# Kernel optimization log

Measured on AMD Instinct MI355X. Metric: run time of the kernel, lower is better.

## Reference

```python
import jax, jax.numpy as jnp
import numpy as np
import math

S, D = 8192, 128

def setup_inputs() -> dict:
    key = jax.random.key(0)
    kq, kk, kv = jax.random.split(key, 3)
    return {
        "q": jax.random.normal(kq, (S, D), dtype=jnp.float32),
        "k": jax.random.normal(kk, (S, D), dtype=jnp.float32),
        "v": jax.random.normal(kv, (S, D), dtype=jnp.float32),
    }

def reference(q, k, v):
    # scores: [S, S]; scale by sqrt(d) as in the torch module
    scale = 1.0 / math.sqrt(q.shape[1])
    scores = (q @ k.T) * scale
    attn = jax.nn.softmax(scores, axis=-1)
    return attn @ v
```

## Files before the change

kernel.cpp:

```cpp
#include <hip/hip_runtime.h>
#include <hip/hip_bf16.h>

#define SEQ 8192
#define HD 128
#define BM 128
#define BN 64
#define NQT (SEQ / BM)
#define THREADS 256
#define KTP 130
#define VTP 66
#define PTP 66

typedef __bf16 bf16_t;
typedef __bf16 bf16x8 __attribute__((ext_vector_type(8)));
typedef float f32x4 __attribute__((ext_vector_type(4)));
typedef float f32x16 __attribute__((ext_vector_type(16)));

#if __has_builtin(__builtin_amdgcn_exp2f)
__device__ inline float exp2_fast(float x) { return __builtin_amdgcn_exp2f(x); }
#else
__device__ inline float exp2_fast(float x) { return exp2f(x); }
#endif

__global__ __launch_bounds__(256) void prep_kernel(const float* __restrict__ K,
                                                   const float* __restrict__ V,
                                                   bf16_t* __restrict__ Kb,
                                                   bf16_t* __restrict__ VT) {
  const int b = (int)blockIdx.x;
  const int tid = (int)threadIdx.x;
  if (b < 256) {
    __shared__ float tile[64][65];
    const int s0 = (b & 127) * 64;
    const int d0 = (b >> 7) * 64;
    const int r = tid >> 2;
    const int c0 = (tid & 3) * 16;
#pragma unroll
    for (int j4 = 0; j4 < 4; ++j4) {
      float4 x = *(const float4*)&V[(size_t)(s0 + r) * HD + d0 + c0 + j4 * 4];
      tile[r][c0 + j4 * 4 + 0] = x.x;
      tile[r][c0 + j4 * 4 + 1] = x.y;
      tile[r][c0 + j4 * 4 + 2] = x.z;
      tile[r][c0 + j4 * 4 + 3] = x.w;
    }
    __syncthreads();
    bf16x8 w0, w1;
#pragma unroll
    for (int j = 0; j < 8; ++j) w0[j] = (bf16_t)tile[c0 + j][r];
#pragma unroll
    for (int j = 0; j < 8; ++j) w1[j] = (bf16_t)tile[c0 + 8 + j][r];
    *(bf16x8*)&VT[(size_t)(d0 + r) * SEQ + s0 + c0] = w0;
    *(bf16x8*)&VT[(size_t)(d0 + r) * SEQ + s0 + c0 + 8] = w1;
  } else {
    const int base = (b - 256) * 2048 + tid * 8;
    float4 a = *(const float4*)&K[base];
    float4 c = *(const float4*)&K[base + 4];
    bf16x8 f;
    f[0] = (bf16_t)a.x; f[1] = (bf16_t)a.y; f[2] = (bf16_t)a.z; f[3] = (bf16_t)a.w;
    f[4] = (bf16_t)c.x; f[5] = (bf16_t)c.y; f[6] = (bf16_t)c.z; f[7] = (bf16_t)c.w;
    *(bf16x8*)&Kb[base] = f;
  }
}

__global__ __launch_bounds__(THREADS, 2) void fattn_kernel(
    const float* __restrict__ Q, const bf16_t* __restrict__ Kb,
    const bf16_t* __restrict__ VT, float* __restrict__ Opart,
    float* __restrict__ Lpart, int kshift, int nit) {
  __shared__ __align__(16) bf16_t kt[BN][KTP];
  __shared__ __align__(16) bf16_t vt[HD][VTP];
  __shared__ __align__(16) bf16_t pt[4][32][PTP];

  const int tid = (int)threadIdx.x;
  const int lane = tid & 63;
  const int w = tid >> 6;
  const int h = lane >> 5;
  const int n32 = lane & 31;

  const int qt = (int)blockIdx.x >> kshift;
  const int sp = (int)blockIdx.x & ((1 << kshift) - 1);
  const int qbase = qt * BM;
  const int kbase0 = sp * (nit * BN);

  const float SC2 = 0.08838834764831845f * 1.4426950408889634f;

  const int kr0 = tid >> 4;
  const int kc8 = (tid & 15) * 8;
  const int vd0 = tid >> 3;
  const int vc8 = (tid & 7) * 8;

  bf16x8 qf[8];
  {
    const float* qp = Q + (size_t)(qbase + w * 32 + n32) * HD + h * 8;
#pragma unroll
    for (int kk = 0; kk < 8; ++kk) {
      float4 a = *(const float4*)(qp + kk * 16);
      float4 b = *(const float4*)(qp + kk * 16 + 4);
      bf16x8 f;
      f[0] = (bf16_t)a.x; f[1] = (bf16_t)a.y; f[2] = (bf16_t)a.z; f[3] = (bf16_t)a.w;
      f[4] = (bf16_t)b.x; f[5] = (bf16_t)b.y; f[6] = (bf16_t)b.z; f[7] = (bf16_t)b.w;
      qf[kk] = f;
    }
  }

  f32x16 o_acc[4];
#pragma unroll
  for (int i = 0; i < 4; ++i)
#pragma unroll
    for (int e = 0; e < 16; ++e) o_acc[i][e] = 0.f;
  float l_acc[16];
#pragma unroll
  for (int i = 0; i < 16; ++i) l_acc[i] = 0.f;

  for (int it = 0; it < nit; ++it) {
    const int kbase = kbase0 + it * BN;

    bf16x8 kreg[4], vreg[4];
#pragma unroll
    for (int j = 0; j < 4; ++j)
      kreg[j] = *(const bf16x8*)&Kb[(size_t)(kbase + kr0 + 16 * j) * HD + kc8];
#pragma unroll
    for (int j = 0; j < 4; ++j)
      vreg[j] = *(const bf16x8*)&VT[(size_t)(vd0 + 32 * j) * SEQ + kbase + vc8];

    __syncthreads();
#pragma unroll
    for (int j = 0; j < 4; ++j) *(bf16x8*)&kt[kr0 + 16 * j][kc8] = kreg[j];
#pragma unroll
    for (int j = 0; j < 4; ++j) *(bf16x8*)&vt[vd0 + 32 * j][vc8] = vreg[j];
    __syncthreads();

    f32x16 sacc[2];
#pragma unroll
    for (int nt = 0; nt < 2; ++nt)
#pragma unroll
      for (int e = 0; e < 16; ++e) sacc[nt][e] = 0.f;
#pragma unroll
    for (int kk = 0; kk < 8; ++kk) {
#pragma unroll
      for (int nt = 0; nt < 2; ++nt) {
        bf16x8 b = *(const bf16x8*)&kt[nt * 32 + n32][kk * 16 + h * 8];
        sacc[nt] = __builtin_amdgcn_mfma_f32_32x32x16_bf16(qf[kk], b, sacc[nt], 0, 0, 0);
      }
    }

#pragma unroll
    for (int nt = 0; nt < 2; ++nt) {
#pragma unroll
      for (int reg = 0; reg < 16; ++reg) {
        float p = exp2_fast(sacc[nt][reg] * SC2);
        l_acc[reg] += p;
        const int row = (reg & 3) + 8 * (reg >> 2);
        pt[w][row + 4 * h][nt * 32 + n32] = (bf16_t)p;
      }
    }

#pragma unroll
    for (int kk = 0; kk < 4; ++kk) {
      bf16x8 pa = *(const bf16x8*)&pt[w][n32][kk * 16 + h * 8];
#pragma unroll
      for (int ot = 0; ot < 4; ++ot) {
        bf16x8 vb = *(const bf16x8*)&vt[ot * 32 + n32][kk * 16 + h * 8];
        o_acc[ot] = __builtin_amdgcn_mfma_f32_32x32x16_bf16(pa, vb, o_acc[ot], 0, 0, 0);
      }
    }
  }

  {
    float* op = Opart + ((size_t)sp * SEQ + qbase + w * 32) * HD;
#pragma unroll
    for (int ot = 0; ot < 4; ++ot)
#pragma unroll
      for (int reg = 0; reg < 16; ++reg) {
        const int row = (reg & 3) + 8 * (reg >> 2) + 4 * h;
        op[row * HD + ot * 32 + n32] = o_acc[ot][reg];
      }
#pragma unroll
    for (int reg = 0; reg < 16; ++reg) {
      float v = l_acc[reg];
      v += __shfl_xor(v, 1);
      v += __shfl_xor(v, 2);
      v += __shfl_xor(v, 4);
      v += __shfl_xor(v, 8);
      v += __shfl_xor(v, 16);
      l_acc[reg] = v;
    }
    if (n32 == 0) {
      float* lp = Lpart + (size_t)sp * SEQ + qbase + w * 32;
#pragma unroll
      for (int reg = 0; reg < 16; ++reg)
        lp[(reg & 3) + 8 * (reg >> 2) + 4 * h] = l_acc[reg];
    }
  }
}

__global__ __launch_bounds__(256) void combine_kernel(const float* __restrict__ Opart,
                                                      const float* __restrict__ Lpart,
                                                      float* __restrict__ out, int ksplit) {
  const int tid = (int)threadIdx.x;
  const int row = (int)blockIdx.x * 8 + (tid >> 5);
  const int c0 = (tid & 31) * 4;
  float lsum = 0.f;
  for (int s = 0; s < ksplit; ++s) lsum += Lpart[(size_t)s * SEQ + row];
  f32x4 acc;
#pragma unroll
  for (int e = 0; e < 4; ++e) acc[e] = 0.f;
  for (int s = 0; s < ksplit; ++s) {
    f32x4 o = *(const f32x4*)&Opart[((size_t)s * SEQ + row) * HD + c0];
#pragma unroll
    for (int e = 0; e < 4; ++e) acc[e] += o[e];
  }
  const float inv = 1.0f / lsum;
  f32x4 res;
#pragma unroll
  for (int e = 0; e < 4; ++e) res[e] = acc[e] * inv;
  *(f32x4*)&out[(size_t)row * HD + c0] = res;
}

extern "C" void kernel_launch(void* const* d_in, const int* in_sizes, int n_in,
                              void* d_out, int out_size, void* d_ws, size_t ws_size,
                              hipStream_t stream) {
  const float* Q = (const float*)d_in[0];
  const float* K = (const float*)d_in[1];
  const float* V = (const float*)d_in[2];
  float* out = (float*)d_out;

  int ksplit = 8, kshift = 3;
  while (ksplit > 1) {
    size_t need = (size_t)ksplit * SEQ * HD * 4
                + (size_t)ksplit * SEQ * 4
                + (size_t)SEQ * HD * 2 * 2;
    if (need <= ws_size) break;
    ksplit >>= 1; kshift--;
  }

  char* ws = (char*)d_ws;
  float* Opart = (float*)ws;
  float* Lpart = (float*)(ws + (size_t)ksplit * SEQ * HD * 4);
  bf16_t* Kb = (bf16_t*)(ws + (size_t)ksplit * SEQ * HD * 4 + (size_t)ksplit * SEQ * 4);
  bf16_t* VT = Kb + (size_t)SEQ * HD;

  const int nit = SEQ / (ksplit * BN);

  prep_kernel<<<768, 256, 0, stream>>>(K, V, Kb, VT);
  fattn_kernel<<<NQT * ksplit, THREADS, 0, stream>>>(Q, Kb, VT, Opart, Lpart, kshift, nit);
  combine_kernel<<<SEQ / 8, 256, 0, stream>>>(Opart, Lpart, out, ksplit);
}
```

Before: 122.6 us.

## Double-buffer K/V tiles and keep P in registers via transposed score MFMA

K and V tiles now live in two LDS buffers. The next tile's global loads are issued before the current tile's compute, leaving one barrier per iteration instead of two. The score MFMA swaps its operands to compute K·Q^T, so each lane holds one query's probabilities. These are packed to bf16 and rearranged with a cross-half lane shuffle to form the PV A-operand directly, which removes the LDS round trip for P and shrinks the row-sum to one value per lane. The softmax scale is folded into Q at load time. In exchange the code adds shuffle and select logic, and the doubled K/V buffers raise LDS use, though the P buffer is gone.

```diff
diff --git a/kernel.cpp b/kernel.cpp
--- a/kernel.cpp
+++ b/kernel.cpp
@@ -9,12 +9,13 @@
 #define THREADS 256
 #define KTP 130
 #define VTP 66
-#define PTP 66
 
 typedef __bf16 bf16_t;
+typedef __bf16 bf16x2 __attribute__((ext_vector_type(2)));
 typedef __bf16 bf16x8 __attribute__((ext_vector_type(8)));
 typedef float f32x4 __attribute__((ext_vector_type(4)));
 typedef float f32x16 __attribute__((ext_vector_type(16)));
+typedef unsigned int u32x4 __attribute__((ext_vector_type(4)));
 
 #if __has_builtin(__builtin_amdgcn_exp2f)
 __device__ inline float exp2_fast(float x) { return __builtin_amdgcn_exp2f(x); }
@@ -65,9 +66,8 @@
     const float* __restrict__ Q, const bf16_t* __restrict__ Kb,
     const bf16_t* __restrict__ VT, float* __restrict__ Opart,
     float* __restrict__ Lpart, int kshift, int nit) {
-  __shared__ __align__(16) bf16_t kt[BN][KTP];
-  __shared__ __align__(16) bf16_t vt[HD][VTP];
-  __shared__ __align__(16) bf16_t pt[4][32][PTP];
+  __shared__ __align__(16) bf16_t kts[2][BN][KTP];
+  __shared__ __align__(16) bf16_t vts[2][HD][VTP];
 
   const int tid = (int)threadIdx.x;
   const int lane = tid & 63;
@@ -95,8 +95,10 @@
       float4 a = *(const float4*)(qp + kk * 16);
       float4 b = *(const float4*)(qp + kk * 16 + 4);
       bf16x8 f;
-      f[0] = (bf16_t)a.x; f[1] = (bf16_t)a.y; f[2] = (bf16_t)a.z; f[3] = (bf16_t)a.w;
-      f[4] = (bf16_t)b.x; f[5] = (bf16_t)b.y; f[6] = (bf16_t)b.z; f[7] = (bf16_t)b.w;
+      f[0] = (bf16_t)(a.x * SC2); f[1] = (bf16_t)(a.y * SC2);
+      f[2] = (bf16_t)(a.z * SC2); f[3] = (bf16_t)(a.w * SC2);
+      f[4] = (bf16_t)(b.x * SC2); f[5] = (bf16_t)(b.y * SC2);
+      f[6] = (bf16_t)(b.z * SC2); f[7] = (bf16_t)(b.w * SC2);
       qf[kk] = f;
     }
   }
@@ -106,62 +108,88 @@
   for (int i = 0; i < 4; ++i)
 #pragma unroll
     for (int e = 0; e < 16; ++e) o_acc[i][e] = 0.f;
-  float l_acc[16];
-#pragma unroll
-  for (int i = 0; i < 16; ++i) l_acc[i] = 0.f;
+  float l_acc = 0.f;
+
+  {
+#pragma unroll
+    for (int j = 0; j < 4; ++j) {
+      bf16x8 kr = *(const bf16x8*)&Kb[(size_t)(kbase0 + kr0 + 16 * j) * HD + kc8];
+      *(bf16x8*)&kts[0][kr0 + 16 * j][kc8] = kr;
+    }
+#pragma unroll
+    for (int j = 0; j < 4; ++j) {
+      bf16x8 vr = *(const bf16x8*)&VT[(size_t)(vd0 + 32 * j) * SEQ + kbase0 + vc8];
+      *(bf16x8*)&vts[0][vd0 + 32 * j][vc8] = vr;
+    }
+  }
+  __syncthreads();
 
   for (int it = 0; it < nit; ++it) {
-    const int kbase = kbase0 + it * BN;
-
+    const int cur = it & 1;
+    const int nxt = cur ^ 1;
+    const int nk = (it + 1 < nit) ? kbase0 + (it + 1) * BN : kbase0;
     bf16x8 kreg[4], vreg[4];
 #pragma unroll
     for (int j = 0; j < 4; ++j)
-      kreg[j] = *(const bf16x8*)&Kb[(size_t)(kbase + kr0 + 16 * j) * HD + kc8];
+      kreg[j] = *(const bf16x8*)&Kb[(size_t)(nk + kr0 + 16 * j) * HD + kc8];
 #pragma unroll
     for (int j = 0; j < 4; ++j)
-      vreg[j] = *(const bf16x8*)&VT[(size_t)(vd0 + 32 * j) * SEQ + kbase + vc8];
-
+      vreg[j] = *(const bf16x8*)&VT[(size_t)(vd0 + 32 * j) * SEQ + nk + vc8];
+
+    f32x16 sacc[2];
+#pragma unroll
+    for (int nt = 0; nt < 2; ++nt)
+#pragma unroll
+      for (int e = 0; e < 16; ++e) sacc[nt][e] = 0.f;
+#pragma unroll
+    for (int kk = 0; kk < 8; ++kk) {
+#pragma unroll
+      for (int nt = 0; nt < 2; ++nt) {
+        bf16x8 af = *(const bf16x8*)&kts[cur][nt * 32 + n32][kk * 16 + h * 8];
+        sacc[nt] = __builtin_amdgcn_mfma_f32_32x32x16_bf16(af, qf[kk], sacc[nt], 0, 0, 0);
+      }
+    }
+
+#pragma unroll
+    for (int nt = 0; nt < 2; ++nt) {
+      float pf[16];
+#pragma unroll
+      for (int r = 0; r < 16; ++r) pf[r] = exp2_fast(sacc[nt][r]);
+#pragma unroll
+      for (int r = 0; r < 16; ++r) l_acc += pf[r];
+      unsigned int pk[8];
+#pragma unroll
+      for (int g = 0; g < 4; ++g) {
+        bf16x2 p0; p0[0] = (bf16_t)pf[4 * g + 0]; p0[1] = (bf16_t)pf[4 * g + 1];
+        bf16x2 p1; p1[0] = (bf16_t)pf[4 * g + 2]; p1[1] = (bf16_t)pf[4 * g + 3];
+        pk[2 * g + 0] = __builtin_bit_cast(unsigned int, p0);
+        pk[2 * g + 1] = __builtin_bit_cast(unsigned int, p1);
+      }
+#pragma unroll
+      for (int kk2 = 0; kk2 < 2; ++kk2) {
+        const unsigned int sA = pk[4 * kk2 + 0], sB = pk[4 * kk2 + 1];
+        const unsigned int sC = pk[4 * kk2 + 2], sD = pk[4 * kk2 + 3];
+        unsigned int s0 = h ? sA : sC, s1 = h ? sB : sD;
+        unsigned int r0 = __shfl_xor(s0, 32);
+        unsigned int r1 = __shfl_xor(s1, 32);
+        unsigned int o0 = h ? sC : sA, o1 = h ? sD : sB;
+        u32x4 fv;
+        fv[0] = h ? r0 : o0; fv[1] = h ? r1 : o1;
+        fv[2] = h ? o0 : r0; fv[3] = h ? o1 : r1;
+        bf16x8 pa = __builtin_bit_cast(bf16x8, fv);
+#pragma unroll
+        for (int ot = 0; ot < 4; ++ot) {
+          bf16x8 vb = *(const bf16x8*)&vts[cur][ot * 32 + n32][nt * 32 + kk2 * 16 + h * 8];
+          o_acc[ot] = __builtin_amdgcn_mfma_f32_32x32x16_bf16(pa, vb, o_acc[ot], 0, 0, 0);
+        }
+      }
+    }
+
+#pragma unroll
+    for (int j = 0; j < 4; ++j) *(bf16x8*)&kts[nxt][kr0 + 16 * j][kc8] = kreg[j];
+#pragma unroll
+    for (int j = 0; j < 4; ++j) *(bf16x8*)&vts[nxt][vd0 + 32 * j][vc8] = vreg[j];
     __syncthreads();
-#pragma unroll
-    for (int j = 0; j < 4; ++j) *(bf16x8*)&kt[kr0 + 16 * j][kc8] = kreg[j];
-#pragma unroll
-    for (int j = 0; j < 4; ++j) *(bf16x8*)&vt[vd0 + 32 * j][vc8] = vreg[j];
-    __syncthreads();
-
-    f32x16 sacc[2];
-#pragma unroll
-    for (int nt = 0; nt < 2; ++nt)
-#pragma unroll
-      for (int e = 0; e < 16; ++e) sacc[nt][e] = 0.f;
-#pragma unroll
-    for (int kk = 0; kk < 8; ++kk) {
-#pragma unroll
-      for (int nt = 0; nt < 2; ++nt) {
-        bf16x8 b = *(const bf16x8*)&kt[nt * 32 + n32][kk * 16 + h * 8];
-        sacc[nt] = __builtin_amdgcn_mfma_f32_32x32x16_bf16(qf[kk], b, sacc[nt], 0, 0, 0);
-      }
-    }
-
-#pragma unroll
-    for (int nt = 0; nt < 2; ++nt) {
-#pragma unroll
-      for (int reg = 0; reg < 16; ++reg) {
-        float p = exp2_fast(sacc[nt][reg] * SC2);
-        l_acc[reg] += p;
-        const int row = (reg & 3) + 8 * (reg >> 2);
-        pt[w][row + 4 * h][nt * 32 + n32] = (bf16_t)p;
-      }
-    }
-
-#pragma unroll
-    for (int kk = 0; kk < 4; ++kk) {
-      bf16x8 pa = *(const bf16x8*)&pt[w][n32][kk * 16 + h * 8];
-#pragma unroll
-      for (int ot = 0; ot < 4; ++ot) {
-        bf16x8 vb = *(const bf16x8*)&vt[ot * 32 + n32][kk * 16 + h * 8];
-        o_acc[ot] = __builtin_amdgcn_mfma_f32_32x32x16_bf16(pa, vb, o_acc[ot], 0, 0, 0);
-      }
-    }
   }
 
   {
@@ -173,22 +201,9 @@
         const int row = (reg & 3) + 8 * (reg >> 2) + 4 * h;
         op[row * HD + ot * 32 + n32] = o_acc[ot][reg];
       }
-#pragma unroll
-    for (int reg = 0; reg < 16; ++reg) {
-      float v = l_acc[reg];
-      v += __shfl_xor(v, 1);
-      v += __shfl_xor(v, 2);
-      v += __shfl_xor(v, 4);
-      v += __shfl_xor(v, 8);
-      v += __shfl_xor(v, 16);
-      l_acc[reg] = v;
-    }
-    if (n32 == 0) {
-      float* lp = Lpart + (size_t)sp * SEQ + qbase + w * 32;
-#pragma unroll
-      for (int reg = 0; reg < 16; ++reg)
-        lp[(reg & 3) + 8 * (reg >> 2) + 4 * h] = l_acc[reg];
-    }
+    float l = l_acc + __shfl_xor(l_acc, 32);
+    if (lane < 32)
+      Lpart[(size_t)sp * SEQ + qbase + w * 32 + n32] = l;
   }
 }
 
```

After: 121.8 us. Within noise of the previous version (-0.6%).
